# Performance work log

Hardware: AMD Instinct MI355X
Metric: run time of the kernel (lower is better)

The kernel has to match this reference:

```python
import jax, jax.numpy as jnp
from jax import lax
import numpy as np

STATE_DIM, H, L = 38000, 32, 3
B, T = 256, 1024


def setup_inputs() -> dict:
    key = jax.random.key(0)
    ks = jax.random.split(key, 16)
    s = 1.0 / np.sqrt(H)
    inp = {
        "x": jax.random.randint(ks[0], (B, T), 0, STATE_DIM, dtype=jnp.int64)
        if jax.config.jax_enable_x64 else jax.random.randint(ks[0], (B, T), 0, STATE_DIM, dtype=jnp.int32),
        "hid": jnp.zeros((L, B, H), dtype=jnp.float32),
        "emb": jax.random.normal(ks[1], (STATE_DIM, H), dtype=jnp.float32),
        "W1": jax.random.uniform(ks[2], (H, H), minval=-s, maxval=s),
        "b1": jax.random.uniform(ks[3], (H,), minval=-s, maxval=s),
        "W2": jax.random.uniform(ks[4], (H, H), minval=-s, maxval=s),
        "b2": jax.random.uniform(ks[5], (H,), minval=-s, maxval=s),
        "W3": jax.random.uniform(ks[6], (H, H), minval=-s, maxval=s),
        "b3": jax.random.uniform(ks[7], (H,), minval=-s, maxval=s),
        # GRU params stacked over layers: gates order (r, z, n) as in PyTorch
        "W_ih": jax.random.uniform(ks[8], (L, 3 * H, H), minval=-s, maxval=s),
        "W_hh": jax.random.uniform(ks[9], (L, 3 * H, H), minval=-s, maxval=s),
        "b_ih": jax.random.uniform(ks[10], (L, 3 * H), minval=-s, maxval=s),
        "b_hh": jax.random.uniform(ks[11], (L, 3 * H), minval=-s, maxval=s),
    }
    return inp


def _gru_layer(x_tbh, h0, W_ih, W_hh, b_ih, b_hh):
    # x_tbh: [T,B,H]; precompute input-side gates once (memory-bound GEMM)
    gi = jnp.einsum('tbh,gh->tbg', x_tbh, W_ih) + b_ih  # [T,B,3H]

    def step(h, gi_t):
        gh = h @ W_hh.T + b_hh  # [B,3H]
        i_r, i_z, i_n = jnp.split(gi_t, 3, axis=-1)
        h_r, h_z, h_n = jnp.split(gh, 3, axis=-1)
        r = jax.nn.sigmoid(i_r + h_r)
        z = jax.nn.sigmoid(i_z + h_z)
        n = jnp.tanh(i_n + r * h_n)
        h_new = (1.0 - z) * n + z * h
        return h_new, h_new

    hT, out = lax.scan(step, h0, gi)
    return out, hT  # [T,B,H], [B,H]


def reference(x, hid, emb, W1, b1, W2, b2, W3, b3, W_ih, W_hh, b_ih, b_hh):
    e = emb[x]  # [B,T,H] embedding lookup
    e = jax.nn.relu(e @ W1.T + b1)
    e = jax.nn.relu(e @ W2.T + b2)
    e = jax.nn.relu(e @ W3.T + b3)
    seq = jnp.transpose(e, (1, 0, 2))  # [T,B,H]
    h_finals = []
    for l in range(L):
        seq, hT = _gru_layer(seq, hid[l], W_ih[l], W_hh[l], b_ih[l], b_hh[l])
        h_finals.append(hT)
    out = jnp.transpose(seq, (1, 0, 2)).reshape(x.shape[0], -1)  # [B, T*H]
    return out, jnp.stack(h_finals, axis=0)
```

## Files before the change

kernel.cpp:

```cpp
#include <hip/hip_runtime.h>

#define BB 256
#define TT 1024
#define HH 32
#define SS 16
#define NBK (TT/SS)
#define NSS (NBK+9)
#define NT 1024
#define SP 32
#define GP 96


__device__ __forceinline__ float fast_rcp(float x) { return __builtin_amdgcn_rcpf(x); }
__device__ __forceinline__ float sigm(float x)     { return fast_rcp(1.f + __expf(-x)); }
__device__ __forceinline__ float tanh_fast(float x){ float e = __expf(2.f * x); return 1.f - 2.f * fast_rcp(e + 1.f); }
__device__ __forceinline__ float rlane(float v, int k) {
    return __int_as_float(__builtin_amdgcn_readlane(__float_as_int(v), k));
}

__global__ __launch_bounds__(NT, 4) void rnn_fused(
    const int*   __restrict__ xidx,
    const float* __restrict__ hid,
    const float* __restrict__ emb,
    const float* __restrict__ W1, const float* __restrict__ b1,
    const float* __restrict__ W2, const float* __restrict__ b2,
    const float* __restrict__ W3, const float* __restrict__ b3,
    const float* __restrict__ Wih,
    const float* __restrict__ Whh,
    const float* __restrict__ bih,
    const float* __restrict__ bhh,
    float*       __restrict__ out)
{
    const int b   = blockIdx.x;
    const int tid = threadIdx.x;
    const int wv  = tid >> 6;
    const int ln  = tid & 63;
    const int lo  = ln & 31;

    __shared__ alignas(16) float ebuf[2][SS][SP];
    __shared__ alignas(16) float y1s [2][SS][SP];
    __shared__ alignas(16) float y2s [2][SS][SP];
    __shared__ alignas(16) float y3s [2][SS][SP];
    __shared__ alignas(16) float h0s [2][SS][SP];
    __shared__ alignas(16) float h1s [2][SS][SP];
    __shared__ alignas(16) float gib [3][2][SS][GP];

    const bool isGH = (wv < 3);
    const bool isY  = (wv >= 4 && wv <= 6);
    const int  ys   = wv - 4;
    const bool isGA = (wv == 9 || wv == 3 || wv == 11);
    const bool isGB = (wv == 10 || wv == 7 || wv == 15);
    const int  gl   = (wv == 9 || wv == 10) ? 0
                    : (wv == 3 || wv == 7)  ? 1 : 2;
    const bool isE  = (wv == 8);

    float wA[32], wB[32];
    float biasA = 0.f, biasB = 0.f, v_h = 0.f;

    if (isGH) {
        const float4* pA = reinterpret_cast<const float4*>(Whh + (size_t)(wv * 96 + ln) * HH);
        const float4* pB = reinterpret_cast<const float4*>(Whh + (size_t)(wv * 96 + 64 + lo) * HH);
        #pragma unroll
        for (int i = 0; i < 8; ++i) {
            reinterpret_cast<float4*>(wA)[i] = pA[i];
            reinterpret_cast<float4*>(wB)[i] = pB[i];
        }
        biasA = bhh[wv * 96 + ln];
        biasB = bhh[wv * 96 + 64 + lo];
        if (ln < HH) v_h = hid[(size_t)(wv * BB + b) * HH + ln];
    } else if (isGA) {
        const float4* pA = reinterpret_cast<const float4*>(Wih + (size_t)(gl * 96 + ln) * HH);
        #pragma unroll
        for (int i = 0; i < 8; ++i) reinterpret_cast<float4*>(wA)[i] = pA[i];
        biasA = bih[gl * 96 + ln];
    } else if (isGB) {
        const float4* pA = reinterpret_cast<const float4*>(Wih + (size_t)(gl * 96 + 64 + lo) * HH);
        #pragma unroll
        for (int i = 0; i < 8; ++i) reinterpret_cast<float4*>(wA)[i] = pA[i];
        biasA = bih[gl * 96 + 64 + lo];
    } else if (isY) {
        const float* Ws = (ys == 0) ? W1 : (ys == 1) ? W2 : W3;
        const float* bs = (ys == 0) ? b1 : (ys == 1) ? b2 : b3;
        const float4* pA = reinterpret_cast<const float4*>(Ws + (size_t)lo * HH);
        #pragma unroll
        for (int i = 0; i < 8; ++i) reinterpret_cast<float4*>(wA)[i] = pA[i];
        biasA = bs[lo];
    }
    __syncthreads();

    float* const out_seq = out + (size_t)b * TT * HH;
    float* const out_hf  = out + (size_t)BB * TT * HH;

    for (int n = 0; n < NSS; ++n) {
        if (isGH) {
            const int blk = n - 5 - 2 * wv;
            if (blk >= 0 && blk < NBK) {
                const int p = blk & 1;
                const float* gsrc = &gib[wv][p][0][0];
                float giA = gsrc[ln];
                float giB = gsrc[64 + lo];
                for (int t2 = 0; t2 < SS; ++t2) {
                    float giA_n = 0.f, giB_n = 0.f;
                    if (t2 + 1 < SS) {
                        giA_n = gsrc[(t2 + 1) * GP + ln];
                        giB_n = gsrc[(t2 + 1) * GP + 64 + lo];
                    }
                    float a0 = biasA, a1 = 0.f, c0 = biasB, c1 = 0.f;
                    #pragma unroll
                    for (int k = 0; k < 32; k += 2) {
                        const float h0 = rlane(v_h, k), h1 = rlane(v_h, k + 1);
                        a0 = fmaf(wA[k],     h0, a0);
                        a1 = fmaf(wA[k + 1], h1, a1);
                        c0 = fmaf(wB[k],     h0, c0);
                        c1 = fmaf(wB[k + 1], h1, c1);
                    }
                    const float sA  = giA + a0 + a1;
                    const float ghB = c0 + c1;
                    const float zp  = __shfl_xor(sA, 32);
                    const float r   = sigm(sA);
                    const float z   = sigm(zp);
                    const float nn  = tanh_fast(fmaf(r, ghB, giB));
                    const float hn  = fmaf(z, v_h - nn, nn);
                    v_h = hn;
                    if (ln < HH) {
                        if (wv == 0)      h0s[p][t2][ln] = hn;
                        else if (wv == 1) h1s[p][t2][ln] = hn;
                        else out_seq[(size_t)(blk * SS + t2) * HH + ln] = hn;
                    }
                    giA = giA_n;
                    giB = giB_n;
                }
            }
        } else if (isGA) {
            const int blk = n - 4 - 2 * gl;
            if (blk >= 0 && blk < NBK) {
                const int p = blk & 1;
                const float* xs = (gl == 0) ? &y3s[p][0][0]
                                : (gl == 1) ? &h0s[p][0][0]
                                            : &h1s[p][0][0];
                float* gdst = &gib[gl][p][0][0];
                for (int t2 = 0; t2 < SS; ++t2) {
                    const float4* xr = reinterpret_cast<const float4*>(xs + t2 * SP);
                    float a0 = biasA, a1 = 0.f, a2 = 0.f, a3 = 0.f;
                    #pragma unroll
                    for (int j = 0; j < 8; ++j) {
                        const float4 xv = xr[j];
                        a0 = fmaf(wA[4 * j + 0], xv.x, a0);
                        a1 = fmaf(wA[4 * j + 1], xv.y, a1);
                        a2 = fmaf(wA[4 * j + 2], xv.z, a2);
                        a3 = fmaf(wA[4 * j + 3], xv.w, a3);
                    }
                    gdst[t2 * GP + ln] = (a0 + a1) + (a2 + a3);
                }
            }
        } else if (isGB) {
            const int blk = n - 4 - 2 * gl;
            if (blk >= 0 && blk < NBK) {
                const int p = blk & 1;
                const float* xs = (gl == 0) ? &y3s[p][0][0]
                                : (gl == 1) ? &h0s[p][0][0]
                                            : &h1s[p][0][0];
                float* gdst = &gib[gl][p][0][0];
                for (int t2 = 0; t2 < SS; ++t2) {
                    const float4* xr = reinterpret_cast<const float4*>(xs + t2 * SP);
                    float a0 = biasA, a1 = 0.f, a2 = 0.f, a3 = 0.f;
                    #pragma unroll
                    for (int j = 0; j < 8; ++j) {
                        const float4 xv = xr[j];
                        a0 = fmaf(wA[4 * j + 0], xv.x, a0);
                        a1 = fmaf(wA[4 * j + 1], xv.y, a1);
                        a2 = fmaf(wA[4 * j + 2], xv.z, a2);
                        a3 = fmaf(wA[4 * j + 3], xv.w, a3);
                    }
                    if (ln < 32) gdst[t2 * GP + 64 + ln] = (a0 + a1) + (a2 + a3);
                }
            }
        } else if (isY) {
            const int blk = n - 1 - ys;
            if (blk >= 0 && blk < NBK) {
                const int p = blk & 1;
                const float* xs = (ys == 0) ? &ebuf[p][0][0]
                                : (ys == 1) ? &y1s[p][0][0]
                                            : &y2s[p][0][0];
                float* dst = (ys == 0) ? &y1s[p][0][0]
                           : (ys == 1) ? &y2s[p][0][0]
                                       : &y3s[p][0][0];
                for (int t2 = 0; t2 < SS; ++t2) {
                    const float4* xr = reinterpret_cast<const float4*>(xs + t2 * SP);
                    float a0 = biasA, a1 = 0.f, a2 = 0.f, a3 = 0.f;
                    #pragma unroll
                    for (int j = 0; j < 8; ++j) {
                        const float4 xv = xr[j];
                        a0 = fmaf(wA[4 * j + 0], xv.x, a0);
                        a1 = fmaf(wA[4 * j + 1], xv.y, a1);
                        a2 = fmaf(wA[4 * j + 2], xv.z, a2);
                        a3 = fmaf(wA[4 * j + 3], xv.w, a3);
                    }
                    const float y = fmaxf((a0 + a1) + (a2 + a3), 0.f);
                    if (ln < 32) dst[t2 * SP + ln] = y;
                }
            }
        } else if (isE) {
            if (n < NBK) {
                const int pe = n & 1, t0 = n * SS;
                #pragma unroll
                for (int k = 0; k < 2; ++k) {
                    const int task = k * 64 + ln;
                    const int row = task >> 3, qq = task & 7;
                    const int tok = xidx[b * TT + t0 + row];
                    const float4 v = *reinterpret_cast<const float4*>(emb + (size_t)tok * HH + qq * 4);
                    *reinterpret_cast<float4*>(&ebuf[pe][row][qq * 4]) = v;
                }
            }
        }
        __syncthreads();
    }

    if (isGH && ln < HH)
        out_hf[(size_t)(wv * BB + b) * HH + ln] = v_h;
}

extern "C" void kernel_launch(void* const* d_in, const int* in_sizes, int n_in,
                              void* d_out, int out_size, void* d_ws, size_t ws_size,
                              hipStream_t stream) {
    const int*   x   = (const int*)  d_in[0];
    const float* hid = (const float*)d_in[1];
    const float* emb = (const float*)d_in[2];
    const float* W1  = (const float*)d_in[3];
    const float* b1  = (const float*)d_in[4];
    const float* W2  = (const float*)d_in[5];
    const float* b2  = (const float*)d_in[6];
    const float* W3  = (const float*)d_in[7];
    const float* b3  = (const float*)d_in[8];
    const float* Wih = (const float*)d_in[9];
    const float* Whh = (const float*)d_in[10];
    const float* bih = (const float*)d_in[11];
    const float* bhh = (const float*)d_in[12];

    rnn_fused<<<dim3(BB), dim3(NT), 0, stream>>>(
        x, hid, emb, W1, b1, W2, b2, W3, b3, Wih, Whh, bih, bhh, (float*)d_out);
}
```

Before: 348.7 us.

## Merge split input-gate waves and shrink block to twelve wavefronts

Each GRU layer's input-gate projection was split across two wavefronts (A rows and B rows); it now runs in a single wavefront holding both weight sets. This cuts the block from 16 to 12 waves (768 threads) with launch bounds of 3, reassigns wave roles, and drops the software prefetch of the next gi values in the recurrent loop. The aim is less barrier and scheduling overhead per stage. The cost is twice the FMA work per input-gate wave, which may lengthen the pipeline stage, plus lower per-block concurrency.

```diff
diff --git a/kernel.cpp b/kernel.cpp
--- a/kernel.cpp
+++ b/kernel.cpp
@@ -6,7 +6,7 @@
 #define SS 16
 #define NBK (TT/SS)
 #define NSS (NBK+9)
-#define NT 1024
+#define NT 768
 #define SP 32
 #define GP 96
 
@@ -18,7 +18,7 @@
     return __int_as_float(__builtin_amdgcn_readlane(__float_as_int(v), k));
 }
 
-__global__ __launch_bounds__(NT, 4) void rnn_fused(
+__global__ __launch_bounds__(NT, 3) void rnn_fused(
     const int*   __restrict__ xidx,
     const float* __restrict__ hid,
     const float* __restrict__ emb,
@@ -46,13 +46,11 @@
     __shared__ alignas(16) float gib [3][2][SS][GP];
 
     const bool isGH = (wv < 3);
-    const bool isY  = (wv >= 4 && wv <= 6);
-    const int  ys   = wv - 4;
-    const bool isGA = (wv == 9 || wv == 3 || wv == 11);
-    const bool isGB = (wv == 10 || wv == 7 || wv == 15);
-    const int  gl   = (wv == 9 || wv == 10) ? 0
-                    : (wv == 3 || wv == 7)  ? 1 : 2;
-    const bool isE  = (wv == 8);
+    const bool isGI = (wv >= 3 && wv < 6);
+    const int  gl   = wv - 3;
+    const bool isY  = (wv >= 6 && wv < 9);
+    const int  ys   = wv - 6;
+    const bool isE  = (wv == 9);
 
     float wA[32], wB[32];
     float biasA = 0.f, biasB = 0.f, v_h = 0.f;
@@ -68,16 +66,16 @@
         biasA = bhh[wv * 96 + ln];
         biasB = bhh[wv * 96 + 64 + lo];
         if (ln < HH) v_h = hid[(size_t)(wv * BB + b) * HH + ln];
-    } else if (isGA) {
+    } else if (isGI) {
         const float4* pA = reinterpret_cast<const float4*>(Wih + (size_t)(gl * 96 + ln) * HH);
+        const float4* pB = reinterpret_cast<const float4*>(Wih + (size_t)(gl * 96 + 64 + lo) * HH);
         #pragma unroll
-        for (int i = 0; i < 8; ++i) reinterpret_cast<float4*>(wA)[i] = pA[i];
+        for (int i = 0; i < 8; ++i) {
+            reinterpret_cast<float4*>(wA)[i] = pA[i];
+            reinterpret_cast<float4*>(wB)[i] = pB[i];
+        }
         biasA = bih[gl * 96 + ln];
-    } else if (isGB) {
-        const float4* pA = reinterpret_cast<const float4*>(Wih + (size_t)(gl * 96 + 64 + lo) * HH);
-        #pragma unroll
-        for (int i = 0; i < 8; ++i) reinterpret_cast<float4*>(wA)[i] = pA[i];
-        biasA = bih[gl * 96 + 64 + lo];
+        biasB = bih[gl * 96 + 64 + lo];
     } else if (isY) {
         const float* Ws = (ys == 0) ? W1 : (ys == 1) ? W2 : W3;
         const float* bs = (ys == 0) ? b1 : (ys == 1) ? b2 : b3;
@@ -97,14 +95,9 @@
             if (blk >= 0 && blk < NBK) {
                 const int p = blk & 1;
                 const float* gsrc = &gib[wv][p][0][0];
-                float giA = gsrc[ln];
-                float giB = gsrc[64 + lo];
                 for (int t2 = 0; t2 < SS; ++t2) {
-                    float giA_n = 0.f, giB_n = 0.f;
-                    if (t2 + 1 < SS) {
-                        giA_n = gsrc[(t2 + 1) * GP + ln];
-                        giB_n = gsrc[(t2 + 1) * GP + 64 + lo];
-                    }
+                    const float giA = gsrc[t2 * GP + ln];
+                    const float giB = gsrc[t2 * GP + 64 + lo];
                     float a0 = biasA, a1 = 0.f, c0 = biasB, c1 = 0.f;
                     #pragma unroll
                     for (int k = 0; k < 32; k += 2) {
@@ -127,11 +120,9 @@
                         else if (wv == 1) h1s[p][t2][ln] = hn;
                         else out_seq[(size_t)(blk * SS + t2) * HH + ln] = hn;
                     }
-                    giA = giA_n;
-                    giB = giB_n;
-                }
-            }
-        } else if (isGA) {
+                }
+            }
+        } else if (isGI) {
             const int blk = n - 4 - 2 * gl;
             if (blk >= 0 && blk < NBK) {
                 const int p = blk & 1;
@@ -142,6 +133,7 @@
                 for (int t2 = 0; t2 < SS; ++t2) {
                     const float4* xr = reinterpret_cast<const float4*>(xs + t2 * SP);
                     float a0 = biasA, a1 = 0.f, a2 = 0.f, a3 = 0.f;
+                    float c0 = biasB, c1 = 0.f, c2 = 0.f, c3 = 0.f;
                     #pragma unroll
                     for (int j = 0; j < 8; ++j) {
                         const float4 xv = xr[j];
@@ -149,30 +141,14 @@
                         a1 = fmaf(wA[4 * j + 1], xv.y, a1);
                         a2 = fmaf(wA[4 * j + 2], xv.z, a2);
                         a3 = fmaf(wA[4 * j + 3], xv.w, a3);
+                        c0 = fmaf(wB[4 * j + 0], xv.x, c0);
+                        c1 = fmaf(wB[4 * j + 1], xv.y, c1);
+                        c2 = fmaf(wB[4 * j + 2], xv.z, c2);
+                        c3 = fmaf(wB[4 * j + 3], xv.w, c3);
                     }
                     gdst[t2 * GP + ln] = (a0 + a1) + (a2 + a3);
-                }
-            }
-        } else if (isGB) {
-            const int blk = n - 4 - 2 * gl;
-            if (blk >= 0 && blk < NBK) {
-                const int p = blk & 1;
-                const float* xs = (gl == 0) ? &y3s[p][0][0]
-                                : (gl == 1) ? &h0s[p][0][0]
-                                            : &h1s[p][0][0];
-                float* gdst = &gib[gl][p][0][0];
-                for (int t2 = 0; t2 < SS; ++t2) {
-                    const float4* xr = reinterpret_cast<const float4*>(xs + t2 * SP);
-                    float a0 = biasA, a1 = 0.f, a2 = 0.f, a3 = 0.f;
-                    #pragma unroll
-                    for (int j = 0; j < 8; ++j) {
-                        const float4 xv = xr[j];
-                        a0 = fmaf(wA[4 * j + 0], xv.x, a0);
-                        a1 = fmaf(wA[4 * j + 1], xv.y, a1);
-                        a2 = fmaf(wA[4 * j + 2], xv.z, a2);
-                        a3 = fmaf(wA[4 * j + 3], xv.w, a3);
-                    }
-                    if (ln < 32) gdst[t2 * GP + 64 + ln] = (a0 + a1) + (a2 + a3);
+                    if (ln < 32)
+                        gdst[t2 * GP + 64 + ln] = (c0 + c1) + (c2 + c3);
                 }
             }
         } else if (isY) {
```

Result: slower. 578.2 us (+65.8%).
